# Optimization experiments

Measured on AMD Instinct MI355X. Metric: run time of the kernel, lower is better.

## Reference

```python
import jax, jax.numpy as jnp
import numpy as np

TEMPERATURE = 10000.0


def _grid_sample_bilinear(img, ix, iy):
    """torch.nn.functional.grid_sample equivalent (bilinear, zero padding,
    align_corners=False), with pixel coords ix, iy already unnormalized.
    img: [B,C,H,W]; ix, iy: [B,K,H,W]. Returns [B,C,K,H,W]."""
    B, C, H, W = img.shape
    K = ix.shape[1]
    x0 = jnp.floor(ix)
    y0 = jnp.floor(iy)
    x1 = x0 + 1.0
    y1 = y0 + 1.0
    wx1 = ix - x0
    wx0 = 1.0 - wx1
    wy1 = iy - y0
    wy0 = 1.0 - wy1
    flat = img.reshape(B, C, H * W)

    def corner(xc, yc, w):
        valid = (xc >= 0) & (xc <= W - 1) & (yc >= 0) & (yc <= H - 1)
        xi = jnp.clip(xc, 0, W - 1).astype(jnp.int32)
        yi = jnp.clip(yc, 0, H - 1).astype(jnp.int32)
        idx = (yi * W + xi).reshape(B, 1, -1)  # [B,1,K*H*W]
        g = jnp.take_along_axis(flat, jnp.broadcast_to(idx, (B, C, idx.shape[-1])), axis=2)
        g = g.reshape(B, C, K, H, W)
        wv = (w * valid.astype(img.dtype)).reshape(B, 1, K, H, W)
        return g * wv

    return (corner(x0, y0, wx0 * wy0) + corner(x1, y0, wx1 * wy0)
            + corner(x0, y1, wx0 * wy1) + corner(x1, y1, wx1 * wy1))


def _forward(left_features, right_features, offset_x, offset_y):
    B, C, H, W = left_features.shape
    dt = left_features.dtype
    # left coordinate grids (buffers built in __init__)
    lx = jnp.arange(W, dtype=dt)[None, None, None, :]               # [1,1,1,W]
    # faithful to original: y coords clamped to max = W-1 (no-op when H<=W)
    ly = jnp.clip(jnp.arange(H, dtype=dt), 0, W - 1)[None, None, :, None]  # [1,1,H,1]

    rx = jnp.clip(lx - offset_x, 0.0, W - 1.0)                      # [B,K,H,W]
    ry = jnp.clip(ly - offset_y, 0.0, H - 1.0)                      # [B,K,H,W]
    # normalize to [-1,1] as in original
    gx = (rx - W / 2) / (W / 2)
    gy = (ry - H / 2) / (H / 2)
    # unnormalize per align_corners=False convention
    ix = ((gx + 1.0) * W - 1.0) * 0.5
    iy = ((gy + 1.0) * H - 1.0) * 0.5

    sampled = _grid_sample_bilinear(right_features, ix, iy)         # [B,C,K,H,W]
    strength = jnp.mean(-jnp.abs(left_features[:, :, None] - sampled), axis=1) * TEMPERATURE  # [B,K,H,W]
    w = jax.nn.softmax(strength, axis=1)
    ox = jnp.sum(offset_x * w, axis=1, keepdims=True)               # [B,1,H,W]
    oy = jnp.sum(offset_y * w, axis=1, keepdims=True)               # [B,1,H,W]
    return ox, oy


def setup_inputs() -> dict:
    key = jax.random.key(0)
    k1, k2, k3, k4 = jax.random.split(key, 4)
    B, C, H, W, K = 1, 32, 256, 512, 10
    left_features = jax.random.normal(k1, (B, C, H, W), jnp.float32)
    right_features = jax.random.normal(k2, (B, C, H, W), jnp.float32)
    # horizontal disparity candidates in [0, 64) px; small vertical jitter
    offset_x = jax.random.uniform(k3, (B, K, H, W), jnp.float32) * 64.0
    offset_y = jax.random.normal(k4, (B, K, H, W), jnp.float32) * 2.0
    return {"left_features": left_features, "right_features": right_features,
            "offset_x": offset_x, "offset_y": offset_y}


def reference(left_features, right_features, offset_x, offset_y):
    return _forward(left_features, right_features, offset_x, offset_y)
```

## Files before the change

kernel.cpp:

```cpp
#include <hip/hip_runtime.h>

constexpr int C = 32, H = 256, W = 512, K = 10;
constexpr int HW = H * W;
constexpr float TEMP = 10000.0f;

__global__ __launch_bounds__(256) void conv_right_hwc(
    const float* __restrict__ in, float* __restrict__ out)
{
    __shared__ float t[C][129];
    const int base = blockIdx.x * 128;
    const int tid = threadIdx.x;
    #pragma unroll
    for (int i = 0; i < 16; ++i) {
        int lin = i * 256 + tid;
        int c = lin >> 7, px = lin & 127;
        t[c][px] = in[c * HW + base + px];
    }
    __syncthreads();
    #pragma unroll
    for (int i = 0; i < 16; ++i) {
        int lin = i * 256 + tid;
        int px = lin >> 5, c = lin & 31;
        out[(base + px) * C + c] = t[c][px];
    }
}

__global__ __launch_bounds__(256, 4) void disp_kernel_hwc(
    const float* __restrict__ lchw, const float* __restrict__ rhwc,
    const float* __restrict__ offx, const float* __restrict__ offy,
    float* __restrict__ out)
{
    const int tid = threadIdx.x;
    const int q = tid & 3;
    const int p = blockIdx.x * 64 + (tid >> 2);
    const int w = p & (W - 1);
    const int h = p >> 9;

    float lf[8];
    #pragma unroll
    for (int j = 0; j < 8; ++j) lf[j] = lchw[(q * 8 + j) * HW + p];

    float okx[K], oky[K];
    #pragma unroll
    for (int k = 0; k < K; ++k) {
        okx[k] = offx[k * HW + p];
        oky[k] = offy[k * HW + p];
    }

    const float lx = (float)w;
    const float ly = (float)h;
    const float4* rbase = (const float4*)rhwc;

    float s[K];

    #pragma unroll
    for (int k = 0; k < K; ++k) {
        const float ox = okx[k];
        const float oy = oky[k];

        float rx = fminf(fmaxf(lx - ox, 0.0f), (float)(W - 1));
        float ry = fminf(fmaxf(ly - oy, 0.0f), (float)(H - 1));
        float gx = (rx - (float)(W / 2)) / (float)(W / 2);
        float gy = (ry - (float)(H / 2)) / (float)(H / 2);
        float ix = ((gx + 1.0f) * (float)W - 1.0f) * 0.5f;
        float iy = ((gy + 1.0f) * (float)H - 1.0f) * 0.5f;

        float x0f = floorf(ix), y0f = floorf(iy);
        float wx1 = ix - x0f, wy1 = iy - y0f;
        float wx0 = 1.0f - wx1, wy0 = 1.0f - wy1;
        int x0 = (int)x0f, y0 = (int)y0f;
        int x1 = x0 + 1,  y1 = y0 + 1;

        float vx0 = (x0 >= 0 && x0 <= W - 1) ? 1.0f : 0.0f;
        float vx1 = (x1 >= 0 && x1 <= W - 1) ? 1.0f : 0.0f;
        float vy0 = (y0 >= 0 && y0 <= H - 1) ? 1.0f : 0.0f;
        float vy1 = (y1 >= 0 && y1 <= H - 1) ? 1.0f : 0.0f;
        float w00 = wx0 * wy0 * vx0 * vy0;
        float w01 = wx1 * wy0 * vx1 * vy0;
        float w10 = wx0 * wy1 * vx0 * vy1;
        float w11 = wx1 * wy1 * vx1 * vy1;

        int xi0 = min(max(x0, 0), W - 1), xi1 = min(max(x1, 0), W - 1);
        int yi0 = min(max(y0, 0), H - 1), yi1 = min(max(y1, 0), H - 1);

        int i00 = (yi0 * W + xi0) * 8 + q * 2;
        int i01 = (yi0 * W + xi1) * 8 + q * 2;
        int i10 = (yi1 * W + xi0) * 8 + q * 2;
        int i11 = (yi1 * W + xi1) * 8 + q * 2;
        float4 a0 = rbase[i00], a1 = rbase[i00 + 1];
        float4 b0 = rbase[i01], b1 = rbase[i01 + 1];
        float4 d0 = rbase[i10], d1 = rbase[i10 + 1];
        float4 e0 = rbase[i11], e1 = rbase[i11 + 1];
        float ca[8] = {a0.x, a0.y, a0.z, a0.w, a1.x, a1.y, a1.z, a1.w};
        float cb[8] = {b0.x, b0.y, b0.z, b0.w, b1.x, b1.y, b1.z, b1.w};
        float cd[8] = {d0.x, d0.y, d0.z, d0.w, d1.x, d1.y, d1.z, d1.w};
        float ce[8] = {e0.x, e0.y, e0.z, e0.w, e1.x, e1.y, e1.z, e1.w};

        float acc = 0.0f;
        #pragma unroll
        for (int j = 0; j < 8; ++j) {
            float g = w00 * ca[j] + w01 * cb[j] + w10 * cd[j] + w11 * ce[j];
            acc += fabsf(lf[j] - g);
        }
        acc += __shfl_xor(acc, 1);
        acc += __shfl_xor(acc, 2);
        s[k] = acc * (-TEMP / (float)C);
    }

    float m = s[0];
    #pragma unroll
    for (int k = 1; k < K; ++k) m = fmaxf(m, s[k]);
    float den = 0.0f, sx = 0.0f, sy = 0.0f;
    #pragma unroll
    for (int k = 0; k < K; ++k) {
        float e = __expf(s[k] - m);
        den += e;
        sx += okx[k] * e;
        sy += oky[k] * e;
    }
    float inv = 1.0f / den;
    if (q == 0) {
        out[p]      = sx * inv;
        out[HW + p] = sy * inv;
    }
}

__global__ __launch_bounds__(256) void disp_kernel_chw(
    const float* __restrict__ left, const float* __restrict__ right,
    const float* __restrict__ offx, const float* __restrict__ offy,
    float* __restrict__ out)
{
    const int p = blockIdx.x * 256 + threadIdx.x;
    const int w = p & (W - 1);
    const int h = p >> 9;
    float lf[C];
    #pragma unroll
    for (int c = 0; c < C; ++c) lf[c] = left[c * HW + p];
    const float lx = (float)w, ly = (float)h;
    float s[K], okx[K], oky[K];
    #pragma unroll
    for (int k = 0; k < K; ++k) {
        const float ox = offx[k * HW + p], oy = offy[k * HW + p];
        okx[k] = ox; oky[k] = oy;
        float rx = fminf(fmaxf(lx - ox, 0.0f), (float)(W - 1));
        float ry = fminf(fmaxf(ly - oy, 0.0f), (float)(H - 1));
        float gx = (rx - 256.0f) / 256.0f, gy = (ry - 128.0f) / 128.0f;
        float ix = ((gx + 1.0f) * (float)W - 1.0f) * 0.5f;
        float iy = ((gy + 1.0f) * (float)H - 1.0f) * 0.5f;
        float x0f = floorf(ix), y0f = floorf(iy);
        float wx1 = ix - x0f, wy1 = iy - y0f;
        float wx0 = 1.0f - wx1, wy0 = 1.0f - wy1;
        int x0 = (int)x0f, y0 = (int)y0f, x1 = x0 + 1, y1 = y0 + 1;
        float vx0 = (x0 >= 0 && x0 <= W - 1) ? 1.0f : 0.0f;
        float vx1 = (x1 >= 0 && x1 <= W - 1) ? 1.0f : 0.0f;
        float vy0 = (y0 >= 0 && y0 <= H - 1) ? 1.0f : 0.0f;
        float vy1 = (y1 >= 0 && y1 <= H - 1) ? 1.0f : 0.0f;
        float w00 = wx0 * wy0 * vx0 * vy0, w01 = wx1 * wy0 * vx1 * vy0;
        float w10 = wx0 * wy1 * vx0 * vy1, w11 = wx1 * wy1 * vx1 * vy1;
        int xi0 = min(max(x0, 0), W - 1), xi1 = min(max(x1, 0), W - 1);
        int yi0 = min(max(y0, 0), H - 1), yi1 = min(max(y1, 0), H - 1);
        int i00 = yi0 * W + xi0, i01 = yi0 * W + xi1;
        int i10 = yi1 * W + xi0, i11 = yi1 * W + xi1;
        float acc = 0.0f;
        #pragma unroll
        for (int c = 0; c < C; ++c) {
            const float* rc = right + c * HW;
            acc += fabsf(lf[c] - (w00 * rc[i00] + w01 * rc[i01]
                                + w10 * rc[i10] + w11 * rc[i11]));
        }
        s[k] = acc * (-TEMP / (float)C);
    }
    float m = s[0];
    #pragma unroll
    for (int k = 1; k < K; ++k) m = fmaxf(m, s[k]);
    float den = 0.0f, sx = 0.0f, sy = 0.0f;
    #pragma unroll
    for (int k = 0; k < K; ++k) {
        float e = __expf(s[k] - m);
        den += e; sx += okx[k] * e; sy += oky[k] * e;
    }
    float inv = 1.0f / den;
    out[p] = sx * inv;
    out[HW + p] = sy * inv;
}

extern "C" void kernel_launch(void* const* d_in, const int* in_sizes, int n_in,
                              void* d_out, int out_size, void* d_ws, size_t ws_size,
                              hipStream_t stream) {
    const float* left  = (const float*)d_in[0];
    const float* right = (const float*)d_in[1];
    const float* offx  = (const float*)d_in[2];
    const float* offy  = (const float*)d_in[3];
    float* out = (float*)d_out;

    const size_t need = (size_t)HW * C * sizeof(float);
    if (ws_size >= need) {
        float* rhwc = (float*)d_ws;
        conv_right_hwc<<<HW / 128, 256, 0, stream>>>(right, rhwc);
        disp_kernel_hwc<<<HW / 64, 256, 0, stream>>>(left, rhwc, offx, offy, out);
    } else {
        disp_kernel_chw<<<HW / 256, 256, 0, stream>>>(left, right, offx, offy, out);
    }
}
```

Baseline: 120.8 us.

## Software-pipeline bilinear gathers across candidates and simplify bounds checks

Restructures the per-candidate loop so the gather loads for candidate k+1 are issued before the loaded values for candidate k are consumed, aiming to hide gather latency. It relies on the clamped coordinate range to drop the upper-bound validity checks and clamps. It also changes the channel split per lane so each quarter-wave reads contiguous float4 chunks at stride 4. The prefetch doubles the live fragment registers, which may hurt occupancy under the launch bound of 4.

```diff
diff --git a/kernel.cpp b/kernel.cpp
--- a/kernel.cpp
+++ b/kernel.cpp
@@ -23,6 +23,60 @@
         int px = lin >> 5, c = lin & 31;
         out[(base + px) * C + c] = t[c][px];
     }
+}
+
+struct Frag {
+    float4 a0, a1, b0, b1, d0, d1, e0, e1;
+    float w00, w01, w10, w11;
+};
+
+__device__ __forceinline__ Frag load_frag(const float4* __restrict__ rb, int q,
+                                          float lx, float ly, float ox, float oy)
+{
+    Frag f;
+    float rx = fminf(fmaxf(lx - ox, 0.0f), (float)(W - 1));
+    float ry = fminf(fmaxf(ly - oy, 0.0f), (float)(H - 1));
+    float gx = (rx - (float)(W / 2)) / (float)(W / 2);
+    float gy = (ry - (float)(H / 2)) / (float)(H / 2);
+    float ix = ((gx + 1.0f) * (float)W - 1.0f) * 0.5f;
+    float iy = ((gy + 1.0f) * (float)H - 1.0f) * 0.5f;
+
+    float x0f = floorf(ix), y0f = floorf(iy);
+    float wx1 = ix - x0f, wy1 = iy - y0f;
+    float wx0 = 1.0f - wx1, wy0 = 1.0f - wy1;
+    int x0 = (int)x0f, y0 = (int)y0f;
+
+    float ax = (x0 >= 0) ? wx0 : 0.0f;
+    float ay = (y0 >= 0) ? wy0 : 0.0f;
+    f.w00 = ax * ay;   f.w01 = wx1 * ay;
+    f.w10 = ax * wy1;  f.w11 = wx1 * wy1;
+
+    int xi0 = max(x0, 0), yi0 = max(y0, 0);
+    int xi1 = x0 + 1,     yi1 = y0 + 1;
+    int r0 = yi0 * W, r1 = yi1 * W;
+    int b00 = (r0 + xi0) * 8 + q;
+    int b01 = (r0 + xi1) * 8 + q;
+    int b10 = (r1 + xi0) * 8 + q;
+    int b11 = (r1 + xi1) * 8 + q;
+    f.a0 = rb[b00]; f.a1 = rb[b00 + 4];
+    f.b0 = rb[b01]; f.b1 = rb[b01 + 4];
+    f.d0 = rb[b10]; f.d1 = rb[b10 + 4];
+    f.e0 = rb[b11]; f.e1 = rb[b11 + 4];
+    return f;
+}
+
+__device__ __forceinline__ float consume(const Frag& f, const float lf[8])
+{
+    float acc = 0.0f;
+    acc += fabsf(lf[0] - (f.w00 * f.a0.x + f.w01 * f.b0.x + f.w10 * f.d0.x + f.w11 * f.e0.x));
+    acc += fabsf(lf[1] - (f.w00 * f.a0.y + f.w01 * f.b0.y + f.w10 * f.d0.y + f.w11 * f.e0.y));
+    acc += fabsf(lf[2] - (f.w00 * f.a0.z + f.w01 * f.b0.z + f.w10 * f.d0.z + f.w11 * f.e0.z));
+    acc += fabsf(lf[3] - (f.w00 * f.a0.w + f.w01 * f.b0.w + f.w10 * f.d0.w + f.w11 * f.e0.w));
+    acc += fabsf(lf[4] - (f.w00 * f.a1.x + f.w01 * f.b1.x + f.w10 * f.d1.x + f.w11 * f.e1.x));
+    acc += fabsf(lf[5] - (f.w00 * f.a1.y + f.w01 * f.b1.y + f.w10 * f.d1.y + f.w11 * f.e1.y));
+    acc += fabsf(lf[6] - (f.w00 * f.a1.z + f.w01 * f.b1.z + f.w10 * f.d1.z + f.w11 * f.e1.z));
+    acc += fabsf(lf[7] - (f.w00 * f.a1.w + f.w01 * f.b1.w + f.w10 * f.d1.w + f.w11 * f.e1.w));
+    return acc;
 }
 
 __global__ __launch_bounds__(256, 4) void disp_kernel_hwc(
@@ -38,7 +92,9 @@
 
     float lf[8];
     #pragma unroll
-    for (int j = 0; j < 8; ++j) lf[j] = lchw[(q * 8 + j) * HW + p];
+    for (int j = 0; j < 4; ++j) lf[j]     = lchw[(4 * q + j) * HW + p];
+    #pragma unroll
+    for (int j = 0; j < 4; ++j) lf[4 + j] = lchw[(16 + 4 * q + j) * HW + p];
 
     float okx[K], oky[K];
     #pragma unroll
@@ -49,62 +105,20 @@
 
     const float lx = (float)w;
     const float ly = (float)h;
-    const float4* rbase = (const float4*)rhwc;
+    const float4* rb = (const float4*)rhwc;
 
     float s[K];
-
-    #pragma unroll
-    for (int k = 0; k < K; ++k) {
-        const float ox = okx[k];
-        const float oy = oky[k];
-
-        float rx = fminf(fmaxf(lx - ox, 0.0f), (float)(W - 1));
-        float ry = fminf(fmaxf(ly - oy, 0.0f), (float)(H - 1));
-        float gx = (rx - (float)(W / 2)) / (float)(W / 2);
-        float gy = (ry - (float)(H / 2)) / (float)(H / 2);
-        float ix = ((gx + 1.0f) * (float)W - 1.0f) * 0.5f;
-        float iy = ((gy + 1.0f) * (float)H - 1.0f) * 0.5f;
-
-        float x0f = floorf(ix), y0f = floorf(iy);
-        float wx1 = ix - x0f, wy1 = iy - y0f;
-        float wx0 = 1.0f - wx1, wy0 = 1.0f - wy1;
-        int x0 = (int)x0f, y0 = (int)y0f;
-        int x1 = x0 + 1,  y1 = y0 + 1;
-
-        float vx0 = (x0 >= 0 && x0 <= W - 1) ? 1.0f : 0.0f;
-        float vx1 = (x1 >= 0 && x1 <= W - 1) ? 1.0f : 0.0f;
-        float vy0 = (y0 >= 0 && y0 <= H - 1) ? 1.0f : 0.0f;
-        float vy1 = (y1 >= 0 && y1 <= H - 1) ? 1.0f : 0.0f;
-        float w00 = wx0 * wy0 * vx0 * vy0;
-        float w01 = wx1 * wy0 * vx1 * vy0;
-        float w10 = wx0 * wy1 * vx0 * vy1;
-        float w11 = wx1 * wy1 * vx1 * vy1;
-
-        int xi0 = min(max(x0, 0), W - 1), xi1 = min(max(x1, 0), W - 1);
-        int yi0 = min(max(y0, 0), H - 1), yi1 = min(max(y1, 0), H - 1);
-
-        int i00 = (yi0 * W + xi0) * 8 + q * 2;
-        int i01 = (yi0 * W + xi1) * 8 + q * 2;
-        int i10 = (yi1 * W + xi0) * 8 + q * 2;
-        int i11 = (yi1 * W + xi1) * 8 + q * 2;
-        float4 a0 = rbase[i00], a1 = rbase[i00 + 1];
-        float4 b0 = rbase[i01], b1 = rbase[i01 + 1];
-        float4 d0 = rbase[i10], d1 = rbase[i10 + 1];
-        float4 e0 = rbase[i11], e1 = rbase[i11 + 1];
-        float ca[8] = {a0.x, a0.y, a0.z, a0.w, a1.x, a1.y, a1.z, a1.w};
-        float cb[8] = {b0.x, b0.y, b0.z, b0.w, b1.x, b1.y, b1.z, b1.w};
-        float cd[8] = {d0.x, d0.y, d0.z, d0.w, d1.x, d1.y, d1.z, d1.w};
-        float ce[8] = {e0.x, e0.y, e0.z, e0.w, e1.x, e1.y, e1.z, e1.w};
-
-        float acc = 0.0f;
-        #pragma unroll
-        for (int j = 0; j < 8; ++j) {
-            float g = w00 * ca[j] + w01 * cb[j] + w10 * cd[j] + w11 * ce[j];
-            acc += fabsf(lf[j] - g);
-        }
+    Frag cur = load_frag(rb, q, lx, ly, okx[0], oky[0]);
+
+    #pragma unroll
+    for (int k = 0; k < K; ++k) {
+        Frag nxt;
+        if (k + 1 < K) nxt = load_frag(rb, q, lx, ly, okx[k + 1], oky[k + 1]);
+        float acc = consume(cur, lf);
         acc += __shfl_xor(acc, 1);
         acc += __shfl_xor(acc, 2);
         s[k] = acc * (-TEMP / (float)C);
+        if (k + 1 < K) cur = nxt;
     }
 
     float m = s[0];
@@ -151,14 +165,12 @@
         float wx1 = ix - x0f, wy1 = iy - y0f;
         float wx0 = 1.0f - wx1, wy0 = 1.0f - wy1;
         int x0 = (int)x0f, y0 = (int)y0f, x1 = x0 + 1, y1 = y0 + 1;
-        float vx0 = (x0 >= 0 && x0 <= W - 1) ? 1.0f : 0.0f;
-        float vx1 = (x1 >= 0 && x1 <= W - 1) ? 1.0f : 0.0f;
-        float vy0 = (y0 >= 0 && y0 <= H - 1) ? 1.0f : 0.0f;
-        float vy1 = (y1 >= 0 && y1 <= H - 1) ? 1.0f : 0.0f;
-        float w00 = wx0 * wy0 * vx0 * vy0, w01 = wx1 * wy0 * vx1 * vy0;
-        float w10 = wx0 * wy1 * vx0 * vy1, w11 = wx1 * wy1 * vx1 * vy1;
-        int xi0 = min(max(x0, 0), W - 1), xi1 = min(max(x1, 0), W - 1);
-        int yi0 = min(max(y0, 0), H - 1), yi1 = min(max(y1, 0), H - 1);
+        float vx0 = (x0 >= 0) ? 1.0f : 0.0f;
+        float vy0 = (y0 >= 0) ? 1.0f : 0.0f;
+        float w00 = wx0 * wy0 * vx0 * vy0, w01 = wx1 * wy0 * vy0;
+        float w10 = wx0 * wy1 * vx0, w11 = wx1 * wy1;
+        int xi0 = max(x0, 0), xi1 = x1;
+        int yi0 = max(y0, 0), yi1 = y1;
         int i00 = yi0 * W + xi0, i01 = yi0 * W + xi1;
         int i10 = yi1 * W + xi0, i11 = yi1 * W + xi1;
         float acc = 0.0f;
```

New measurement: 122.8 us. No clear change (+1.7%).
